# Kernel tuning notes

Hardware: AMD Instinct MI355X
Metric: run time of the kernel (lower is better)

Reference implementation:

```python
import jax, jax.numpy as jnp
import numpy as np

N_NODES = 40000
N_EDGES = 640000
DIM = 128
N_BASIS = 50
N_FILTERS = 128
CUTOFF = 5.0
LOG2 = float(np.log(2.0))
PI = float(np.pi)


def ssp(t):
    # ShiftedSoftplus: softplus(x) - log(2), numerically stable via logaddexp
    return jnp.logaddexp(t, 0.0) - LOG2


def setup_inputs() -> dict:
    key = jax.random.key(0)
    ks = jax.random.split(key, 16)
    u = lambda k, shape, fan_in: jax.random.uniform(k, shape, jnp.float32, -1.0, 1.0) / np.sqrt(fan_in)
    return {
        "x": jax.random.normal(ks[0], (N_NODES, DIM), jnp.float32),
        "r_ij": jax.random.uniform(ks[1], (N_EDGES,), jnp.float32) * CUTOFF,
        "f_ij": jax.random.normal(ks[2], (N_EDGES, N_BASIS), jnp.float32),
        "ind_i": jax.random.randint(ks[3], (N_EDGES,), 0, N_NODES),
        "ind_j": jax.random.randint(ks[4], (N_EDGES,), 0, N_NODES),
        # parameters
        "W_in2f": u(ks[5], (DIM, N_FILTERS), DIM),            # Linear(dim, n_filters, bias=False)
        "W_f1": u(ks[6], (N_BASIS, N_FILTERS), N_BASIS),       # filter_network Linear 1
        "b_f1": u(ks[7], (N_FILTERS,), N_BASIS),
        "W_f2": u(ks[8], (N_FILTERS, N_FILTERS), N_FILTERS),   # filter_network Linear 2
        "b_f2": u(ks[9], (N_FILTERS,), N_FILTERS),
        "W_out": u(ks[10], (N_FILTERS, DIM), N_FILTERS),       # f2out Linear
        "b_out": u(ks[11], (DIM,), N_FILTERS),
        "W_lin": u(ks[12], (DIM, DIM), DIM),                   # final lin
        "b_lin": u(ks[13], (DIM,), DIM),
    }


def reference(x, r_ij, f_ij, ind_i, ind_j,
              W_in2f, W_f1, b_f1, W_f2, b_f2, W_out, b_out, W_lin, b_lin):
    # filter network: Linear -> ShiftedSoftplus -> Linear, on edges: [E, nf]
    W = ssp(f_ij @ W_f1 + b_f1) @ W_f2 + b_f2
    # cosine cutoff: [E]
    C = 0.5 * (jnp.cos(r_ij * (PI / CUTOFF)) + 1.0) * (r_ij < CUTOFF).astype(r_ij.dtype)
    W = W * C[:, None]
    # node embedding -> filters: [N, nf]
    h = x @ W_in2f
    # gather source nodes, modulate by filters: [E, nf]
    msg = h[ind_j] * W
    # scatter-add pool to destination nodes: [N, nf]
    agg = jax.ops.segment_sum(msg, ind_i, num_segments=x.shape[0])
    # f2out: Linear -> ShiftedSoftplus, then final Linear
    v = ssp(agg @ W_out + b_out)
    return v @ W_lin + b_lin
```

## Files before the change

kernel.cpp:

```cpp
#include <hip/hip_runtime.h>
#include <hip/hip_fp16.h>

#define N_NODES_C 40000
#define N_EDGES_C 640000
#define DIM 128
#define NB 50
#define LDA 132
#define BLK 256
#define TROWS 64
#define LOG2_C 0.6931471805599453f
#define PI_OVER_CUT 0.6283185307179586f
#define NSCAN_BLK 157

typedef __attribute__((ext_vector_type(8))) short s8v;
typedef __attribute__((ext_vector_type(4))) float f4v;

#define MFMA_BF16 __builtin_amdgcn_mfma_f32_16x16x32_bf16

#define SEG_IN2F_H 0
#define SEG_IN2F_L 20480
#define SEG_F1_H   40960
#define SEG_F1_L   51200
#define SEG_F2_H   61440
#define SEG_F2_L   81920
#define SEG_OUT_H  102400
#define SEG_OUT_L  122880
#define SEG_LIN_H  143360
#define SEG_LIN_L  163840
#define WSPLIT_USHORTS 184320

__device__ __forceinline__ unsigned short f2bf(float x) {
    unsigned int u = __float_as_uint(x);
    u += 0x7fffu + ((u >> 16) & 1u);
    return (unsigned short)(u >> 16);
}
__device__ __forceinline__ float bf2f(unsigned short h) {
    return __uint_as_float(((unsigned int)h) << 16);
}
__device__ __forceinline__ float ssp_f(float t) {
    float e = __expf(-fabsf(t));
    return fmaxf(t, 0.0f) + __logf(1.0f + e) - LOG2_C;
}
__device__ __forceinline__ void split8t(const float* av, s8v& Ah, s8v& Al) {
#pragma unroll
    for (int j = 0; j < 8; j += 2) {
        unsigned int u0 = __float_as_uint(av[j]);
        unsigned int u1 = __float_as_uint(av[j + 1]);
        float h0 = __uint_as_float(u0 & 0xffff0000u);
        float h1 = __uint_as_float(u1 & 0xffff0000u);
        unsigned int r0 = __float_as_uint(av[j] - h0);
        unsigned int r1 = __float_as_uint(av[j + 1] - h1);
        ((unsigned int*)&Ah)[j >> 1] = __builtin_amdgcn_perm(u1, u0, 0x07060302);
        ((unsigned int*)&Al)[j >> 1] = __builtin_amdgcn_perm(r1, r0, 0x07060302);
    }
}
__device__ __forceinline__ void f2x4_to_split(const float2 v[4], s8v& Ah, s8v& Al) {
    float av[8] = {v[0].x, v[0].y, v[1].x, v[1].y, v[2].x, v[2].y, v[3].x, v[3].y};
    split8t(av, Ah, Al);
}
__device__ __forceinline__ void loadB4(const unsigned short* __restrict__ p, s8v B[4]) {
#pragma unroll
    for (int t = 0; t < 4; ++t) B[t] = *(const s8v*)(p + t * 640);
}
__device__ __forceinline__ void mfma8_half(const s8v B[4], const s8v& A0, const s8v& A1,
                                           f4v acc0[4], f4v acc1[4]) {
#pragma unroll
    for (int t = 0; t < 4; ++t) {
        acc0[t] = MFMA_BF16(A0, B[t], acc0[t], 0, 0, 0);
        acc1[t] = MFMA_BF16(A1, B[t], acc1[t], 0, 0, 0);
    }
}
__device__ __forceinline__ void mfma16_half(const s8v B[4], const s8v& Ah0, const s8v& Al0,
                                            const s8v& Ah1, const s8v& Al1,
                                            f4v acc0[4], f4v acc1[4]) {
#pragma unroll
    for (int t = 0; t < 4; ++t) {
        acc0[t] = MFMA_BF16(Al0, B[t], acc0[t], 0, 0, 0);
        acc0[t] = MFMA_BF16(Ah0, B[t], acc0[t], 0, 0, 0);
        acc1[t] = MFMA_BF16(Al1, B[t], acc1[t], 0, 0, 0);
        acc1[t] = MFMA_BF16(Ah1, B[t], acc1[t], 0, 0, 0);
    }
}
__device__ __forceinline__ void mfma4x2(const unsigned short* __restrict__ bh,
                                        const unsigned short* __restrict__ bl,
                                        const s8v& Ah0, const s8v& Al0,
                                        const s8v& Ah1, const s8v& Al1,
                                        f4v acc0[4], f4v acc1[4]) {
    s8v B[4];
    loadB4(bl, B);
    mfma8_half(B, Ah0, Ah1, acc0, acc1);
    loadB4(bh, B);
    mfma16_half(B, Ah0, Al0, Ah1, Al1, acc0, acc1);
}
__device__ __forceinline__ void init_acc_cols(f4v acc0[4], f4v acc1[4],
                                              const float* __restrict__ b, int colbase, int lr) {
#pragma unroll
    for (int t = 0; t < 4; ++t) {
        float bv = b[colbase + t * 16 + lr];
        acc0[t] = (f4v){bv, bv, bv, bv};
        acc1[t] = (f4v){bv, bv, bv, bv};
    }
}
__device__ __forceinline__ void gemm_lds_ws(const unsigned short* __restrict__ t1h,
                                            const unsigned short* __restrict__ t1l,
                                            int rowA0, int rowA1, int lk,
                                            const unsigned short* __restrict__ bh,
                                            const unsigned short* __restrict__ bl,
                                            f4v acc0[4], f4v acc1[4]) {
#pragma unroll
    for (int kc = 0; kc < 4; ++kc) {
        s8v Ah0 = *(const s8v*)&t1h[rowA0 * 136 + kc * 32 + lk * 8];
        s8v Al0 = *(const s8v*)&t1l[rowA0 * 136 + kc * 32 + lk * 8];
        s8v Ah1 = *(const s8v*)&t1h[rowA1 * 136 + kc * 32 + lk * 8];
        s8v Al1 = *(const s8v*)&t1l[rowA1 * 136 + kc * 32 + lk * 8];
        s8v B[4];
        loadB4(bl + kc * 5120, B);
        mfma8_half(B, Ah0, Ah1, acc0, acc1);
        loadB4(bh + kc * 5120, B);
        mfma16_half(B, Ah0, Al0, Ah1, Al1, acc0, acc1);
    }
}
__device__ __forceinline__ void store_t1_ssp(const f4v acc0[4], const f4v acc1[4],
                                             unsigned short* __restrict__ t1h,
                                             unsigned short* __restrict__ t1l,
                                             int rpair, int colbase, int lk, int lr) {
#pragma unroll
    for (int t = 0; t < 4; ++t)
#pragma unroll
        for (int r = 0; r < 4; ++r) {
            int col = colbase + t * 16 + lr;
            float v = ssp_f(acc0[t][r]);
            unsigned int u = __float_as_uint(v);
            float hf = __uint_as_float(u & 0xffff0000u);
            int idx = (rpair * 32 + lk * 4 + r) * 136 + col;
            t1h[idx] = (unsigned short)(u >> 16);
            t1l[idx] = (unsigned short)(__float_as_uint(v - hf) >> 16);
            v = ssp_f(acc1[t][r]);
            u = __float_as_uint(v);
            hf = __uint_as_float(u & 0xffff0000u);
            idx = (rpair * 32 + 16 + lk * 4 + r) * 136 + col;
            t1h[idx] = (unsigned short)(u >> 16);
            t1l[idx] = (unsigned short)(__float_as_uint(v - hf) >> 16);
        }
}

__global__ __launch_bounds__(BLK) void split5_kernel(const float* __restrict__ Wa,
                                                     const float* __restrict__ Wb,
                                                     const float* __restrict__ Wc,
                                                     const float* __restrict__ Wd,
                                                     const float* __restrict__ We,
                                                     unsigned short* __restrict__ Ws) {
    int i = blockIdx.x * BLK + threadIdx.x;
    if (i >= 18 * 4096) return;
    int chunk = i >> 12, r = i & 4095, k = r & 31, col = r >> 5;
    const float* W; int Kr, ck, hb, lb;
    if (chunk < 4)       { W = Wa; Kr = 128; ck = chunk;      hb = SEG_IN2F_H; lb = SEG_IN2F_L; }
    else if (chunk < 6)  { W = Wb; Kr = 50;  ck = chunk - 4;  hb = SEG_F1_H;   lb = SEG_F1_L; }
    else if (chunk < 10) { W = Wc; Kr = 128; ck = chunk - 6;  hb = SEG_F2_H;   lb = SEG_F2_L; }
    else if (chunk < 14) { W = Wd; Kr = 128; ck = chunk - 10; hb = SEG_OUT_H;  lb = SEG_OUT_L; }
    else                 { W = We; Kr = 128; ck = chunk - 14; hb = SEG_LIN_H;  lb = SEG_LIN_L; }
    int krow = ck * 32 + k;
    float v = (krow < Kr) ? W[(size_t)krow * DIM + col] : 0.f;
    unsigned short h16 = f2bf(v);
    int o = ck * 5120 + col * 40 + k;
    Ws[hb + o] = h16;
    Ws[lb + o] = f2bf(v - bf2f(h16));
}

__global__ __launch_bounds__(BLK, 4) void node_in2f_mfma(const float* __restrict__ x,
                                                         const unsigned short* __restrict__ Ws,
                                                         float* __restrict__ h) {
    const int tid = threadIdx.x;
    const int w = tid >> 6, l = tid & 63, lr = l & 15, lk = l >> 4;
    const int rpair = w & 1, colbase = (w >> 1) * 64;
    const int n0 = blockIdx.x * TROWS;
    const int rowA0 = rpair * 32 + lr, rowA1 = rowA0 + 16;
    const float* xr0 = x + (size_t)(n0 + rowA0) * DIM;
    const float* xr1 = x + (size_t)(n0 + rowA1) * DIM;

    f4v acc0[4], acc1[4];
#pragma unroll
    for (int t = 0; t < 4; ++t) {
        acc0[t] = (f4v){0.f, 0.f, 0.f, 0.f};
        acc1[t] = (f4v){0.f, 0.f, 0.f, 0.f};
    }
#pragma unroll
    for (int kc = 0; kc < 4; ++kc) {
        const float* ap0 = xr0 + kc * 32 + lk * 8;
        const float* ap1 = xr1 + kc * 32 + lk * 8;
        float4 a0 = *(const float4*)ap0, a1 = *(const float4*)(ap0 + 4);
        float4 b0 = *(const float4*)ap1, b1 = *(const float4*)(ap1 + 4);
        float av0[8] = {a0.x, a0.y, a0.z, a0.w, a1.x, a1.y, a1.z, a1.w};
        float av1[8] = {b0.x, b0.y, b0.z, b0.w, b1.x, b1.y, b1.z, b1.w};
        s8v Ah0, Al0, Ah1, Al1;
        split8t(av0, Ah0, Al0);
        split8t(av1, Ah1, Al1);
        const int bo = kc * 5120 + (colbase + lr) * 40 + lk * 8;
        mfma4x2(Ws + SEG_IN2F_H + bo, Ws + SEG_IN2F_L + bo, Ah0, Al0, Ah1, Al1, acc0, acc1);
    }
#pragma unroll
    for (int t = 0; t < 4; ++t)
#pragma unroll
        for (int r = 0; r < 4; ++r) {
            int col = colbase + t * 16 + lr;
            h[(size_t)(n0 + rpair * 32 + lk * 4 + r) * DIM + col] = acc0[t][r];
            h[(size_t)(n0 + rpair * 32 + 16 + lk * 4 + r) * DIM + col] = acc1[t][r];
        }
}

__global__ __launch_bounds__(BLK) void hist_kernel(const int* __restrict__ ind_i,
                                                   int* __restrict__ cnt) {
    int e = blockIdx.x * BLK + threadIdx.x;
    if (e < N_EDGES_C) atomicAdd(&cnt[ind_i[e]], 1);
}

__global__ __launch_bounds__(BLK) void scan1_kernel(const int* __restrict__ cnt,
                                                    int* __restrict__ excl,
                                                    int* __restrict__ bsum) {
    __shared__ int s[BLK];
    const int tid = threadIdx.x;
    const int idx = blockIdx.x * BLK + tid;
    int v = (idx < N_NODES_C) ? cnt[idx] : 0;
    s[tid] = v;
    __syncthreads();
    for (int off = 1; off < BLK; off <<= 1) {
        int t = (tid >= off) ? s[tid - off] : 0;
        __syncthreads();
        s[tid] += t;
        __syncthreads();
    }
    if (idx < N_NODES_C) excl[idx] = s[tid] - v;
    if (tid == BLK - 1) bsum[blockIdx.x] = s[tid];
}

__global__ __launch_bounds__(BLK) void scan2_kernel(int* __restrict__ bsum) {
    __shared__ int s[BLK];
    const int tid = threadIdx.x;
    int v = (tid < NSCAN_BLK) ? bsum[tid] : 0;
    s[tid] = v;
    __syncthreads();
    for (int off = 1; off < BLK; off <<= 1) {
        int t = (tid >= off) ? s[tid - off] : 0;
        __syncthreads();
        s[tid] += t;
        __syncthreads();
    }
    if (tid < NSCAN_BLK) bsum[tid] = s[tid] - v;
}

__global__ __launch_bounds__(BLK) void scan3_kernel(int* __restrict__ start,
                                                    int* __restrict__ cursor,
                                                    const int* __restrict__ bsum) {
    const int idx = blockIdx.x * BLK + threadIdx.x;
    if (idx < N_NODES_C) {
        int v = start[idx] + bsum[blockIdx.x];
        start[idx] = v;
        cursor[idx] = v;
    }
}

__global__ __launch_bounds__(BLK) void place_kernel(const int* __restrict__ ind_i,
                                                    int* __restrict__ cursor,
                                                    int* __restrict__ pos) {
    int e = blockIdx.x * BLK + threadIdx.x;
    if (e < N_EDGES_C) {
        int slot = atomicAdd(&cursor[ind_i[e]], 1);
        pos[e] = slot;
    }
}

__global__ __launch_bounds__(BLK, 5) void edge_kernel_mfma(const float* __restrict__ f_ij,
                                                           const float* __restrict__ r_ij,
                                                           const int* __restrict__ ind_j,
                                                           const int* __restrict__ pos,
                                                           const unsigned short* __restrict__ Ws,
                                                           const float* __restrict__ b_f1,
                                                           const float* __restrict__ b_f2,
                                                           const float* __restrict__ h,
                                                           __half* __restrict__ msg) {
    __shared__ __align__(16) char smem[17408];
    unsigned short* t1b = (unsigned short*)smem;
    __half* tfh = (__half*)smem;

    const int tid = threadIdx.x;
    const int w = tid >> 6, l = tid & 63, lr = l & 15, lk = l >> 4;
    const int rt = tid >> 4, ct = tid & 15;
    const int rpair = w & 1, colbase = (w >> 1) * 64;
    const int e0 = blockIdx.x * TROWS;
    const int rowA0 = rpair * 32 + lr, rowA1 = rowA0 + 16;
    const int boff = (colbase + lr) * 40 + lk * 8;

    f4v acc0[4], acc1[4];
    init_acc_cols(acc0, acc1, b_f1, colbase, lr);
    const float* fr0 = f_ij + (size_t)(e0 + rowA0) * NB;
    const float* fr1 = f_ij + (size_t)(e0 + rowA1) * NB;
    const unsigned short* f1h = Ws + SEG_F1_H + boff;
    const unsigned short* f1l = Ws + SEG_F1_L + boff;
#pragma unroll
    for (int kc = 0; kc < 2; ++kc) {
        float2 v0[4], v1[4];
#pragma unroll
        for (int ii = 0; ii < 4; ++ii) {
            int k = kc * 32 + lk * 8 + ii * 2;
            v0[ii] = (k < NB) ? *(const float2*)(fr0 + k) : make_float2(0.f, 0.f);
            v1[ii] = (k < NB) ? *(const float2*)(fr1 + k) : make_float2(0.f, 0.f);
        }
        s8v Ah0, Al0, Ah1, Al1;
        f2x4_to_split(v0, Ah0, Al0);
        f2x4_to_split(v1, Ah1, Al1);
        s8v B[4];
        loadB4(f1l + kc * 5120, B);
        mfma8_half(B, Ah0, Ah1, acc0, acc1);
        loadB4(f1h + kc * 5120, B);
        mfma16_half(B, Ah0, Al0, Ah1, Al1, acc0, acc1);
    }
#pragma unroll
    for (int t = 0; t < 4; ++t)
#pragma unroll
        for (int r = 0; r < 4; ++r) {
            int col = colbase + t * 16 + lr;
            t1b[(rpair * 32 + lk * 4 + r) * 136 + col] = f2bf(ssp_f(acc0[t][r]));
            t1b[(rpair * 32 + 16 + lk * 4 + r) * 136 + col] = f2bf(ssp_f(acc1[t][r]));
        }
    __syncthreads();

    init_acc_cols(acc0, acc1, b_f2, colbase, lr);
    const unsigned short* f2h = Ws + SEG_F2_H + boff;
    const unsigned short* f2l = Ws + SEG_F2_L + boff;
#pragma unroll
    for (int kc = 0; kc < 4; ++kc) {
        s8v Ab0 = *(const s8v*)&t1b[rowA0 * 136 + kc * 32 + lk * 8];
        s8v Ab1 = *(const s8v*)&t1b[rowA1 * 136 + kc * 32 + lk * 8];
        s8v B[4];
        loadB4(f2l + kc * 5120, B);
        mfma8_half(B, Ab0, Ab1, acc0, acc1);
        loadB4(f2h + kc * 5120, B);
        mfma8_half(B, Ab0, Ab1, acc0, acc1);
    }
    __syncthreads();
#pragma unroll
    for (int t = 0; t < 4; ++t)
#pragma unroll
        for (int r = 0; r < 4; ++r) {
            int col = colbase + t * 16 + lr;
            tfh[(rpair * 32 + lk * 4 + r) * 136 + col] = __float2half_rn(acc0[t][r]);
            tfh[(rpair * 32 + 16 + lk * 4 + r) * 136 + col] = __float2half_rn(acc1[t][r]);
        }
    __syncthreads();

#pragma unroll
    for (int i = 0; i < 4; ++i) {
        int e = e0 + rt * 4 + i;
        float rr = r_ij[e];
        float C = (rr < 5.0f) ? (0.5f * __cosf(rr * PI_OVER_CUT) + 0.5f) : 0.0f;
        int nj = ind_j[e];
        const __half* ep = &tfh[(rt * 4 + i) * 136 + ct * 8];
        uint4 av = *(const uint4*)ep;
        const __half2* ah2 = (const __half2*)&av;
        const float* hp = &h[(size_t)nj * DIM + ct * 8];
        float4 h0 = *(const float4*)hp, h1 = *(const float4*)(hp + 4);
        float2 a01 = __half22float2(ah2[0]), a23 = __half22float2(ah2[1]);
        float2 a45 = __half22float2(ah2[2]), a67 = __half22float2(ah2[3]);
        __half2 o0 = __floats2half2_rn(h0.x * a01.x * C, h0.y * a01.y * C);
        __half2 o1 = __floats2half2_rn(h0.z * a23.x * C, h0.w * a23.y * C);
        __half2 o2 = __floats2half2_rn(h1.x * a45.x * C, h1.y * a45.y * C);
        __half2 o3 = __floats2half2_rn(h1.z * a67.x * C, h1.w * a67.y * C);
        __half* mp = &msg[(size_t)pos[e] * DIM + ct * 8];
        *(uint4*)mp = make_uint4(*(unsigned int*)&o0, *(unsigned int*)&o1,
                                 *(unsigned int*)&o2, *(unsigned int*)&o3);
    }
}

__global__ __launch_bounds__(BLK, 4) void node_out_fused(const __half* __restrict__ msg,
                                                         const int* __restrict__ start,
                                                         const int* __restrict__ cnt,
                                                         const unsigned short* __restrict__ Ws,
                                                         const float* __restrict__ b_out,
                                                         const float* __restrict__ b_lin,
                                                         float* __restrict__ out) {
    __shared__ __align__(16) char smem[34816];
    unsigned short* t1h = (unsigned short*)smem;
    unsigned short* t1l = t1h + 64 * 136;

    const int tid = threadIdx.x;
    const int w = tid >> 6, l = tid & 63, lr = l & 15, lk = l >> 4;
    const int rpair = w & 1, colbase = (w >> 1) * 64;
    const int n0 = blockIdx.x * TROWS;
    const int rowA0 = rpair * 32 + lr, rowA1 = rowA0 + 16;
    const int boff = (colbase + lr) * 40 + lk * 8;

    const int q = tid >> 4, l16 = tid & 15;
#pragma unroll
    for (int i = 0; i < 4; ++i) {
        int nrow = q * 4 + i;
        int node = n0 + nrow;
        int s = start[node];
        int d = cnt[node];
        float a[8] = {0.f, 0.f, 0.f, 0.f, 0.f, 0.f, 0.f, 0.f};
        const __half* bp = msg + (size_t)s * DIM + l16 * 8;
        for (int k = 0; k < d; ++k) {
            uint4 v = *(const uint4*)(bp + (size_t)k * DIM);
            const __half2* hp2 = (const __half2*)&v;
#pragma unroll
            for (int j = 0; j < 4; ++j) {
                float2 f = __half22float2(hp2[j]);
                a[j * 2] += f.x;
                a[j * 2 + 1] += f.y;
            }
        }
        s8v Ah, Al;
        split8t(a, Ah, Al);
        *(s8v*)&t1h[nrow * 136 + l16 * 8] = Ah;
        *(s8v*)&t1l[nrow * 136 + l16 * 8] = Al;
    }
    __syncthreads();

    f4v acc0[4], acc1[4];
    init_acc_cols(acc0, acc1, b_out, colbase, lr);
    gemm_lds_ws(t1h, t1l, rowA0, rowA1, lk,
                Ws + SEG_OUT_H + boff, Ws + SEG_OUT_L + boff, acc0, acc1);
    __syncthreads();
    store_t1_ssp(acc0, acc1, t1h, t1l, rpair, colbase, lk, lr);
    __syncthreads();

    init_acc_cols(acc0, acc1, b_lin, colbase, lr);
    gemm_lds_ws(t1h, t1l, rowA0, rowA1, lk,
                Ws + SEG_LIN_H + boff, Ws + SEG_LIN_L + boff, acc0, acc1);
#pragma unroll
    for (int t = 0; t < 4; ++t)
#pragma unroll
        for (int r = 0; r < 4; ++r) {
            int col = colbase + t * 16 + lr;
            out[(size_t)(n0 + rpair * 32 + lk * 4 + r) * DIM + col] = acc0[t][r];
            out[(size_t)(n0 + rpair * 32 + 16 + lk * 4 + r) * DIM + col] = acc1[t][r];
        }
}

__device__ __forceinline__ void stage_chunk(const float* __restrict__ B, int k0, int rows,
                                            float* __restrict__ Bc, int tid) {
    const int n4 = rows * (DIM / 4);
    const float4* Bg = (const float4*)B + (size_t)k0 * (DIM / 4);
    float4* Bc4 = (float4*)Bc;
    for (int i = tid; i < n4; i += BLK) Bc4[i] = Bg[i];
}

__device__ __forceinline__ void init_acc_bias(float acc[4][8], const float* __restrict__ b, int ct) {
    float4 bb0 = *(const float4*)&b[ct * 8];
    float4 bb1 = *(const float4*)&b[ct * 8 + 4];
#pragma unroll
    for (int i = 0; i < 4; ++i) {
        acc[i][0] = bb0.x; acc[i][1] = bb0.y; acc[i][2] = bb0.z; acc[i][3] = bb0.w;
        acc[i][4] = bb1.x; acc[i][5] = bb1.y; acc[i][6] = bb1.z; acc[i][7] = bb1.w;
    }
}

template <int KPAD>
__device__ __forceinline__ void gemm_tile(const float* __restrict__ A_lds, int lda,
                                          const float* __restrict__ Bglob,
                                          float* __restrict__ Bc,
                                          float acc[4][8], int rt, int ct, int tid) {
    for (int k0 = 0; k0 < KPAD; k0 += 32) {
        __syncthreads();
        stage_chunk(Bglob, k0, 32, Bc, tid);
        __syncthreads();
#pragma unroll 2
        for (int k4 = 0; k4 < 8; ++k4) {
            float4 av[4];
#pragma unroll
            for (int i = 0; i < 4; ++i)
                av[i] = *(const float4*)&A_lds[(rt * 4 + i) * lda + k0 + k4 * 4];
#pragma unroll
            for (int kk = 0; kk < 4; ++kk) {
                const float* bp = &Bc[(k4 * 4 + kk) * DIM + ct * 8];
                float4 b0 = *(const float4*)bp;
                float4 b1 = *(const float4*)(bp + 4);
#pragma unroll
                for (int i = 0; i < 4; ++i) {
                    float a = ((const float*)&av[i])[kk];
                    acc[i][0] = fmaf(a, b0.x, acc[i][0]);
                    acc[i][1] = fmaf(a, b0.y, acc[i][1]);
                    acc[i][2] = fmaf(a, b0.z, acc[i][2]);
                    acc[i][3] = fmaf(a, b0.w, acc[i][3]);
                    acc[i][4] = fmaf(a, b1.x, acc[i][4]);
                    acc[i][5] = fmaf(a, b1.y, acc[i][5]);
                    acc[i][6] = fmaf(a, b1.z, acc[i][6]);
                    acc[i][7] = fmaf(a, b1.w, acc[i][7]);
                }
            }
        }
    }
}

template <int NK2>
__device__ __forceinline__ void gemm1_direct(const float* const (&frow)[4], int k2base,
                                             const float* __restrict__ Bc,
                                             float acc[4][8], int ct) {
#pragma unroll 4
    for (int k2 = 0; k2 < NK2; ++k2) {
        float2 a2[4];
#pragma unroll
        for (int i = 0; i < 4; ++i)
            a2[i] = *(const float2*)(frow[i] + (k2base + k2) * 2);
#pragma unroll
        for (int kk = 0; kk < 2; ++kk) {
            const float* bp = &Bc[(k2 * 2 + kk) * DIM + ct * 8];
            float4 b0 = *(const float4*)bp;
            float4 b1 = *(const float4*)(bp + 4);
#pragma unroll
            for (int i = 0; i < 4; ++i) {
                float a = kk ? a2[i].y : a2[i].x;
                acc[i][0] = fmaf(a, b0.x, acc[i][0]);
                acc[i][1] = fmaf(a, b0.y, acc[i][1]);
                acc[i][2] = fmaf(a, b0.z, acc[i][2]);
                acc[i][3] = fmaf(a, b0.w, acc[i][3]);
                acc[i][4] = fmaf(a, b1.x, acc[i][4]);
                acc[i][5] = fmaf(a, b1.y, acc[i][5]);
                acc[i][6] = fmaf(a, b1.z, acc[i][6]);
                acc[i][7] = fmaf(a, b1.w, acc[i][7]);
            }
        }
    }
}

__global__ __launch_bounds__(BLK) void node_in2f_fb(const float* __restrict__ x,
                                                    const float* __restrict__ W,
                                                    float* __restrict__ h) {
    __shared__ float At[TROWS * LDA];
    __shared__ float Bc[32 * DIM];
    const int tid = threadIdx.x;
    const int rt = tid >> 4, ct = tid & 15;
    const int n0 = blockIdx.x * TROWS;
    for (int i = tid; i < TROWS * (DIM / 4); i += BLK) {
        int row = i >> 5, c4 = i & 31;
        *(float4*)&At[row * LDA + c4 * 4] = *(const float4*)&x[(size_t)(n0 + row) * DIM + c4 * 4];
    }
    float acc[4][8];
#pragma unroll
    for (int i = 0; i < 4; ++i)
#pragma unroll
        for (int j = 0; j < 8; ++j) acc[i][j] = 0.f;
    gemm_tile<DIM>(At, LDA, W, Bc, acc, rt, ct, tid);
#pragma unroll
    for (int i = 0; i < 4; ++i) {
        float* hp = &h[(size_t)(n0 + rt * 4 + i) * DIM + ct * 8];
        *(float4*)hp = make_float4(acc[i][0], acc[i][1], acc[i][2], acc[i][3]);
        *(float4*)(hp + 4) = make_float4(acc[i][4], acc[i][5], acc[i][6], acc[i][7]);
    }
}

__global__ __launch_bounds__(BLK) void node_out_fb(const float* __restrict__ agg,
                                                   const float* __restrict__ W_out,
                                                   const float* __restrict__ b_out,
                                                   const float* __restrict__ W_lin,
                                                   const float* __restrict__ b_lin,
                                                   float* __restrict__ out) {
    __shared__ float At[TROWS * LDA];
    __shared__ float Bc[32 * DIM];
    const int tid = threadIdx.x;
    const int rt = tid >> 4, ct = tid & 15;
    const int n0 = blockIdx.x * TROWS;
    for (int i = tid; i < TROWS * (DIM / 4); i += BLK) {
        int row = i >> 5, c4 = i & 31;
        *(float4*)&At[row * LDA + c4 * 4] = *(const float4*)&agg[(size_t)(n0 + row) * DIM + c4 * 4];
    }
    float acc[4][8];
    init_acc_bias(acc, b_out, ct);
    gemm_tile<DIM>(At, LDA, W_out, Bc, acc, rt, ct, tid);
    __syncthreads();
#pragma unroll
    for (int i = 0; i < 4; ++i) {
        float* tp = &At[(rt * 4 + i) * LDA + ct * 8];
        *(float4*)tp = make_float4(ssp_f(acc[i][0]), ssp_f(acc[i][1]),
                                   ssp_f(acc[i][2]), ssp_f(acc[i][3]));
        *(float4*)(tp + 4) = make_float4(ssp_f(acc[i][4]), ssp_f(acc[i][5]),
                                         ssp_f(acc[i][6]), ssp_f(acc[i][7]));
    }
    init_acc_bias(acc, b_lin, ct);
    gemm_tile<DIM>(At, LDA, W_lin, Bc, acc, rt, ct, tid);
#pragma unroll
    for (int i = 0; i < 4; ++i) {
        float* op = &out[(size_t)(n0 + rt * 4 + i) * DIM + ct * 8];
        *(float4*)op = make_float4(acc[i][0], acc[i][1], acc[i][2], acc[i][3]);
        *(float4*)(op + 4) = make_float4(acc[i][4], acc[i][5], acc[i][6], acc[i][7]);
    }
}

__global__ __launch_bounds__(BLK) void edge_kernel_atomic(const float* __restrict__ f_ij,
                                                          const float* __restrict__ r_ij,
                                                          const int* __restrict__ ind_i,
                                                          const int* __restrict__ ind_j,
                                                          const float* __restrict__ W_f1,
                                                          const float* __restrict__ b_f1,
                                                          const float* __restrict__ W_f2,
                                                          const float* __restrict__ b_f2,
                                                          const float* __restrict__ h,
                                                          float* __restrict__ agg) {
    __shared__ float t1[TROWS * LDA];
    __shared__ float Bc[32 * DIM];
    const int tid = threadIdx.x;
    const int rt = tid >> 4, ct = tid & 15;
    const int e0 = blockIdx.x * TROWS;
    const float* frow[4];
#pragma unroll
    for (int i = 0; i < 4; ++i) frow[i] = f_ij + (size_t)(e0 + rt * 4 + i) * NB;
    float acc[4][8];
    init_acc_bias(acc, b_f1, ct);
    stage_chunk(W_f1, 0, 32, Bc, tid);
    __syncthreads();
    gemm1_direct<16>(frow, 0, Bc, acc, ct);
    __syncthreads();
    stage_chunk(W_f1, 32, 18, Bc, tid);
    __syncthreads();
    gemm1_direct<9>(frow, 16, Bc, acc, ct);
#pragma unroll
    for (int i = 0; i < 4; ++i) {
        float* tp = &t1[(rt * 4 + i) * LDA + ct * 8];
        *(float4*)tp = make_float4(ssp_f(acc[i][0]), ssp_f(acc[i][1]),
                                   ssp_f(acc[i][2]), ssp_f(acc[i][3]));
        *(float4*)(tp + 4) = make_float4(ssp_f(acc[i][4]), ssp_f(acc[i][5]),
                                         ssp_f(acc[i][6]), ssp_f(acc[i][7]));
    }
    init_acc_bias(acc, b_f2, ct);
    gemm_tile<DIM>(t1, LDA, W_f2, Bc, acc, rt, ct, tid);
#pragma unroll
    for (int i = 0; i < 4; ++i) {
        int e = e0 + rt * 4 + i;
        float r = r_ij[e];
        float C = (r < 5.0f) ? 0.5f * (cosf(r * PI_OVER_CUT) + 1.0f) : 0.0f;
        int nj = ind_j[e];
        int ni = ind_i[e];
        const float* hp = &h[(size_t)nj * DIM + ct * 8];
        float4 h0 = *(const float4*)hp;
        float4 h1 = *(const float4*)(hp + 4);
        float* ap = &agg[(size_t)ni * DIM + ct * 8];
        atomicAdd(ap + 0, h0.x * acc[i][0] * C);
        atomicAdd(ap + 1, h0.y * acc[i][1] * C);
        atomicAdd(ap + 2, h0.z * acc[i][2] * C);
        atomicAdd(ap + 3, h0.w * acc[i][3] * C);
        atomicAdd(ap + 4, h1.x * acc[i][4] * C);
        atomicAdd(ap + 5, h1.y * acc[i][5] * C);
        atomicAdd(ap + 6, h1.z * acc[i][6] * C);
        atomicAdd(ap + 7, h1.w * acc[i][7] * C);
    }
}

extern "C" void kernel_launch(void* const* d_in, const int* in_sizes, int n_in,
                              void* d_out, int out_size, void* d_ws, size_t ws_size,
                              hipStream_t stream) {
    const float* x      = (const float*)d_in[0];
    const float* r_ij   = (const float*)d_in[1];
    const float* f_ij   = (const float*)d_in[2];
    const int*   ind_i  = (const int*)d_in[3];
    const int*   ind_j  = (const int*)d_in[4];
    const float* W_in2f = (const float*)d_in[5];
    const float* W_f1   = (const float*)d_in[6];
    const float* b_f1   = (const float*)d_in[7];
    const float* W_f2   = (const float*)d_in[8];
    const float* b_f2   = (const float*)d_in[9];
    const float* W_out  = (const float*)d_in[10];
    const float* b_out  = (const float*)d_in[11];
    const float* W_lin  = (const float*)d_in[12];
    const float* b_lin  = (const float*)d_in[13];
    float* out = (float*)d_out;

    char* ws = (char*)d_ws;
    size_t off = 0;
    auto alloc = [&](size_t bytes) {
        char* p = ws + off;
        off = (off + bytes + 511) & ~(size_t)511;
        return p;
    };
    unsigned short* Wsplit = (unsigned short*)alloc(WSPLIT_USHORTS * sizeof(unsigned short));
    float*  h      = (float*)alloc((size_t)N_NODES_C * DIM * sizeof(float));
    __half* msg    = (__half*)alloc((size_t)N_EDGES_C * DIM * sizeof(__half));
    int*    pos    = (int*)alloc((size_t)N_EDGES_C * sizeof(int));
    int*    cnt    = (int*)alloc((size_t)N_NODES_C * sizeof(int));
    int*    startA = (int*)alloc((size_t)N_NODES_C * sizeof(int));
    int*    cursor = (int*)alloc((size_t)N_NODES_C * sizeof(int));
    int*    bsum   = (int*)alloc((size_t)NSCAN_BLK * sizeof(int));
    const bool have_ws = (off <= ws_size);

    if (have_ws) {
        split5_kernel<<<(18 * 4096 + BLK - 1) / BLK, BLK, 0, stream>>>(
            W_in2f, W_f1, W_f2, W_out, W_lin, Wsplit);

        node_in2f_mfma<<<N_NODES_C / TROWS, BLK, 0, stream>>>(x, Wsplit, h);

        hipMemsetAsync(cnt, 0, (size_t)N_NODES_C * sizeof(int), stream);
        hist_kernel<<<(N_EDGES_C + BLK - 1) / BLK, BLK, 0, stream>>>(ind_i, cnt);
        scan1_kernel<<<NSCAN_BLK, BLK, 0, stream>>>(cnt, startA, bsum);
        scan2_kernel<<<1, BLK, 0, stream>>>(bsum);
        scan3_kernel<<<NSCAN_BLK, BLK, 0, stream>>>(startA, cursor, bsum);
        place_kernel<<<(N_EDGES_C + BLK - 1) / BLK, BLK, 0, stream>>>(ind_i, cursor, pos);

        edge_kernel_mfma<<<N_EDGES_C / TROWS, BLK, 0, stream>>>(
            f_ij, r_ij, ind_j, pos, Wsplit, b_f1, b_f2, h, msg);

        node_out_fused<<<N_NODES_C / TROWS, BLK, 0, stream>>>(
            msg, startA, cnt, Wsplit, b_out, b_lin, out);
    } else {
        float* h2   = (float*)d_ws;
        float* agg2 = h2 + (size_t)N_NODES_C * DIM;
        node_in2f_fb<<<N_NODES_C / TROWS, BLK, 0, stream>>>(x, W_in2f, h2);
        hipMemsetAsync(agg2, 0, (size_t)N_NODES_C * DIM * sizeof(float), stream);
        edge_kernel_atomic<<<N_EDGES_C / TROWS, BLK, 0, stream>>>(
            f_ij, r_ij, ind_i, ind_j, W_f1, b_f1, W_f2, b_f2, h2, agg2);
        node_out_fb<<<N_NODES_C / TROWS, BLK, 0, stream>>>(agg2, W_out, b_out, W_lin, b_lin, out);
    }
}
```

Baseline: 299.7 us.

## Remap edge-kernel MFMA warp tiling to 64 rows x 32 cols per wave

Each wave in the edge filter-network kernel now covers all 64 edge rows and a 32-column slice, instead of a 32-row by 64-column tile. The aim is to halve the weight B-fragment loads per wave and reuse each B fragment across four row tiles. In exchange every wave must read and split all 64 rows of f_ij and read all 64 rows of t1 from LDS. That multiplies the redundant global f_ij reads and split work across waves.

Result: no change. 304.7 us (+1.7%).

```diff
diff --git a/kernel.cpp b/kernel.cpp
--- a/kernel.cpp
+++ b/kernel.cpp
@@ -62,6 +62,10 @@
 #pragma unroll
     for (int t = 0; t < 4; ++t) B[t] = *(const s8v*)(p + t * 640);
 }
+__device__ __forceinline__ void loadB2(const unsigned short* __restrict__ p, s8v B[2]) {
+    B[0] = *(const s8v*)p;
+    B[1] = *(const s8v*)(p + 640);
+}
 __device__ __forceinline__ void mfma8_half(const s8v B[4], const s8v& A0, const s8v& A1,
                                            f4v acc0[4], f4v acc1[4]) {
 #pragma unroll
@@ -91,6 +95,13 @@
     mfma8_half(B, Ah0, Ah1, acc0, acc1);
     loadB4(bh, B);
     mfma16_half(B, Ah0, Al0, Ah1, Al1, acc0, acc1);
+}
+__device__ __forceinline__ void mfma42(const s8v B[2], const s8v A[4], f4v acc[4][2]) {
+#pragma unroll
+    for (int rt4 = 0; rt4 < 4; ++rt4)
+#pragma unroll
+        for (int t = 0; t < 2; ++t)
+            acc[rt4][t] = MFMA_BF16(A[rt4], B[t], acc[rt4][t], 0, 0, 0);
 }
 __device__ __forceinline__ void init_acc_cols(f4v acc0[4], f4v acc1[4],
                                               const float* __restrict__ b, int colbase, int lr) {
@@ -285,67 +296,79 @@
     const int tid = threadIdx.x;
     const int w = tid >> 6, l = tid & 63, lr = l & 15, lk = l >> 4;
     const int rt = tid >> 4, ct = tid & 15;
-    const int rpair = w & 1, colbase = (w >> 1) * 64;
+    const int colbase = w * 32;
     const int e0 = blockIdx.x * TROWS;
-    const int rowA0 = rpair * 32 + lr, rowA1 = rowA0 + 16;
     const int boff = (colbase + lr) * 40 + lk * 8;
 
-    f4v acc0[4], acc1[4];
-    init_acc_cols(acc0, acc1, b_f1, colbase, lr);
-    const float* fr0 = f_ij + (size_t)(e0 + rowA0) * NB;
-    const float* fr1 = f_ij + (size_t)(e0 + rowA1) * NB;
+    f4v acc[4][2];
+#pragma unroll
+    for (int t = 0; t < 2; ++t) {
+        float bv = b_f1[colbase + t * 16 + lr];
+#pragma unroll
+        for (int rt4 = 0; rt4 < 4; ++rt4) acc[rt4][t] = (f4v){bv, bv, bv, bv};
+    }
     const unsigned short* f1h = Ws + SEG_F1_H + boff;
     const unsigned short* f1l = Ws + SEG_F1_L + boff;
 #pragma unroll
     for (int kc = 0; kc < 2; ++kc) {
-        float2 v0[4], v1[4];
-#pragma unroll
-        for (int ii = 0; ii < 4; ++ii) {
-            int k = kc * 32 + lk * 8 + ii * 2;
-            v0[ii] = (k < NB) ? *(const float2*)(fr0 + k) : make_float2(0.f, 0.f);
-            v1[ii] = (k < NB) ? *(const float2*)(fr1 + k) : make_float2(0.f, 0.f);
+        s8v Ah[4], Al[4];
+#pragma unroll
+        for (int rt4 = 0; rt4 < 4; ++rt4) {
+            const float* fr = f_ij + (size_t)(e0 + rt4 * 16 + lr) * NB;
+            float2 v[4];
+#pragma unroll
+            for (int ii = 0; ii < 4; ++ii) {
+                int k = kc * 32 + lk * 8 + ii * 2;
+                v[ii] = (k < NB) ? *(const float2*)(fr + k) : make_float2(0.f, 0.f);
+            }
+            f2x4_to_split(v, Ah[rt4], Al[rt4]);
         }
-        s8v Ah0, Al0, Ah1, Al1;
-        f2x4_to_split(v0, Ah0, Al0);
-        f2x4_to_split(v1, Ah1, Al1);
-        s8v B[4];
-        loadB4(f1l + kc * 5120, B);
-        mfma8_half(B, Ah0, Ah1, acc0, acc1);
-        loadB4(f1h + kc * 5120, B);
-        mfma16_half(B, Ah0, Al0, Ah1, Al1, acc0, acc1);
-    }
-#pragma unroll
-    for (int t = 0; t < 4; ++t)
-#pragma unroll
-        for (int r = 0; r < 4; ++r) {
-            int col = colbase + t * 16 + lr;
-            t1b[(rpair * 32 + lk * 4 + r) * 136 + col] = f2bf(ssp_f(acc0[t][r]));
-            t1b[(rpair * 32 + 16 + lk * 4 + r) * 136 + col] = f2bf(ssp_f(acc1[t][r]));
-        }
-    __syncthreads();
-
-    init_acc_cols(acc0, acc1, b_f2, colbase, lr);
+        s8v B[2];
+        loadB2(f1l + kc * 5120, B);
+        mfma42(B, Ah, acc);
+        loadB2(f1h + kc * 5120, B);
+        mfma42(B, Al, acc);
+        mfma42(B, Ah, acc);
+    }
+#pragma unroll
+    for (int rt4 = 0; rt4 < 4; ++rt4)
+#pragma unroll
+        for (int t = 0; t < 2; ++t)
+#pragma unroll
+            for (int r = 0; r < 4; ++r)
+                t1b[(rt4 * 16 + lk * 4 + r) * 136 + colbase + t * 16 + lr] =
+                    f2bf(ssp_f(acc[rt4][t][r]));
+    __syncthreads();
+
+#pragma unroll
+    for (int t = 0; t < 2; ++t) {
+        float bv = b_f2[colbase + t * 16 + lr];
+#pragma unroll
+        for (int rt4 = 0; rt4 < 4; ++rt4) acc[rt4][t] = (f4v){bv, bv, bv, bv};
+    }
     const unsigned short* f2h = Ws + SEG_F2_H + boff;
     const unsigned short* f2l = Ws + SEG_F2_L + boff;
 #pragma unroll
     for (int kc = 0; kc < 4; ++kc) {
-        s8v Ab0 = *(const s8v*)&t1b[rowA0 * 136 + kc * 32 + lk * 8];
-        s8v Ab1 = *(const s8v*)&t1b[rowA1 * 136 + kc * 32 + lk * 8];
-        s8v B[4];
-        loadB4(f2l + kc * 5120, B);
-        mfma8_half(B, Ab0, Ab1, acc0, acc1);
-        loadB4(f2h + kc * 5120, B);
-        mfma8_half(B, Ab0, Ab1, acc0, acc1);
-    }
-    __syncthreads();
-#pragma unroll
-    for (int t = 0; t < 4; ++t)
-#pragma unroll
-        for (int r = 0; r < 4; ++r) {
-            int col = colbase + t * 16 + lr;
-            tfh[(rpair * 32 + lk * 4 + r) * 136 + col] = __float2half_rn(acc0[t][r]);
-            tfh[(rpair * 32 + 16 + lk * 4 + r) * 136 + col] = __float2half_rn(acc1[t][r]);
-        }
+        s8v Ab[4];
+#pragma unroll
+        for (int rt4 = 0; rt4 < 4; ++rt4)
+            Ab[rt4] = *(const s8v*)&t1b[(rt4 * 16 + lr) * 136 + kc * 32 + lk * 8];
+        s8v B[2];
+        loadB2(f2l + kc * 5120, B);
+        mfma42(B, Ab, acc);
+        loadB2(f2h + kc * 5120, B);
+        mfma42(B, Ab, acc);
+    }
+    __syncthreads();
+#pragma unroll
+    for (int rt4 = 0; rt4 < 4; ++rt4)
+#pragma unroll
+        for (int t = 0; t < 2; ++t)
+#pragma unroll
+            for (int r = 0; r < 4; ++r)
+                tfh[(rt4 * 16 + lk * 4 + r) * 136 + colbase + t * 16 + lr] =
+                    __float2half_rn(acc[rt4][t][r]);
     __syncthreads();
 
 #pragma unroll
```
